# Performance work log

Measured on AMD Instinct MI355X. Metric: run time of the kernel, lower is better.

## Reference

```python
import jax, jax.numpy as jnp
import numpy as np
from jax import lax

CHAOS_R = 3.5699456
N_STEPS = 10


def setup_inputs() -> dict:
    key = jax.random.key(0)
    k1, k2, k3 = jax.random.split(key, 3)
    B, T, D = 256, 8192, 5
    x = jax.random.normal(k1, (B, T, D), dtype=jnp.float32)
    temple = jax.random.normal(k2, (4, 5), dtype=jnp.float32)
    breath_vector = jax.random.normal(k3, (5,), dtype=jnp.float32)
    return {"x": x, "temple": temple, "breath_vector": breath_vector}


def reference(x, temple, breath_vector):
    # x: (B, T, D) with D == 5
    B, T, D = x.shape

    # mirror_sequence: chaos logistic map on mean of x[0,0]
    seed = jnp.mod(jnp.mean(x[0, 0]), 1.0)
    chaos = CHAOS_R * seed * (1.0 - seed)
    mirrored = jnp.where(chaos > 0.7, 9.0 - x,
                         jnp.where(chaos > 0.4, jnp.flip(x, axis=1), x))
    mode_code = jnp.where(chaos > 0.7, 0, jnp.where(chaos > 0.4, 1, 2))  # 0=invert,1=retrograde,2=none

    extended_x = jnp.concatenate([x, mirrored], axis=1)  # (B, 2T, D)

    # per-token breath: first T tokens use breath[:4], mirrored half uses breath[1:5]
    breath_main = breath_vector[:4]
    breath_mirror = breath_vector[1:5]
    breath = jnp.concatenate([
        jnp.broadcast_to(breath_main, (T, 4)),
        jnp.broadcast_to(breath_mirror, (T, 4)),
    ], axis=0)  # (2T, 4)

    def step(vec, _):
        # vec: (B, 2T, 5)
        transformed = jnp.einsum('rd,btd->btr', temple, vec)  # (B, 2T, 4)
        resonance = jnp.sum(transformed * breath[None, :, :], axis=-1)  # (B, 2T)
        vec = jnp.roll(vec, shift=1, axis=-1).at[..., 0].set(jnp.mod(resonance, 10.0))
        return vec, resonance

    vec0 = extended_x[..., :5]
    _, history = lax.scan(step, vec0, None, length=N_STEPS)  # (10, B, 2T)

    # torch.std default is unbiased (ddof=1)
    score = 1.0 / (1.0 + jnp.std(history, axis=0, ddof=1))  # (B, 2T)
    gate_weights = score[..., None]  # (B, 2T, 1)
    return gate_weights, extended_x, mode_code
```

## Files before the change

### kernel.cpp

```cpp
#include <hip/hip_runtime.h>

#define NSTEPS 10
constexpr int B_DIM = 256, T_DIM = 8192, D_DIM = 5;
constexpr int TILE  = 1024;
constexpr int BLOCK = 256;
constexpr long long GATE_N = (long long)B_DIM * 2 * T_DIM;
constexpr long long EXT_N  = GATE_N * D_DIM;

__device__ __forceinline__ float scan_score(double v0, double v1, double v2, double v3, double v4,
                                            const double* __restrict__ w) {
    float h[NSTEPS];
#pragma unroll
    for (int s = 0; s < NSTEPS; ++s) {
        double res = v0 * w[0];
        res = fma(v1, w[1], res);
        res = fma(v2, w[2], res);
        res = fma(v3, w[3], res);
        res = fma(v4, w[4], res);
        h[s] = (float)res;
        double q = floor(res * 0.1);
        double m = fma(q, -10.0, res);
        m = (m < 0.0)   ? m + 10.0 : m;
        m = (m >= 10.0) ? m - 10.0 : m;
        v4 = v3; v3 = v2; v2 = v1; v1 = v0; v0 = m;
    }
    float mean = 0.f;
#pragma unroll
    for (int s = 0; s < NSTEPS; ++s) mean += h[s];
    mean *= 0.1f;
    float ssd = 0.f;
#pragma unroll
    for (int s = 0; s < NSTEPS; ++s) { float d = h[s] - mean; ssd = fmaf(d, d, ssd); }
    float sd = sqrtf(ssd * (1.0f / 9.0f));
    return 1.0f / (1.0f + sd);
}

__global__ __launch_bounds__(BLOCK) void temple_gate_kernel(
    const float* __restrict__ x, const float* __restrict__ temple,
    const float* __restrict__ breath, float* __restrict__ out) {
    __shared__ float lds[TILE * D_DIM];

    const int k  = threadIdx.x;
    const int b  = blockIdx.x >> 3;
    const int t0 = (blockIdx.x & 7) * TILE;

    double s = 0.0;
    for (int d = 0; d < 5; ++d) s += (double)x[d];
    s = s / 5.0;
    double seed  = s - floor(s);
    double chaos = 3.5699456 * seed * (1.0 - seed);
    const int mode = (chaos > 0.7) ? 0 : ((chaos > 0.4) ? 1 : 2);
    double wm[5], wx[5];
#pragma unroll
    for (int d = 0; d < 5; ++d) {
        double a = 0.0, c = 0.0;
#pragma unroll
        for (int r = 0; r < 4; ++r) {
            double tv = (double)temple[r * 5 + d];
            a += (double)breath[r]     * tv;
            c += (double)breath[r + 1] * tv;
        }
        wm[d] = a; wx[d] = c;
    }
    if (blockIdx.x == 0 && k == 0) out[GATE_N + EXT_N] = (float)mode;

    const long long srcBase = ((long long)b * T_DIM + t0) * D_DIM;
    const float4* __restrict__ src = (const float4*)(x + srcBase);
    float4 r0 = src[k],       r1 = src[k + 256], r2 = src[k + 512],
           r3 = src[k + 768], r4 = src[k + 1024];

    float4* l4 = (float4*)lds;
    l4[k] = r0; l4[k + 256] = r1; l4[k + 512] = r2; l4[k + 768] = r3; l4[k + 1024] = r4;

    float* gate = out;
    float* ext  = out + GATE_N;
    const long long rowBase = (long long)b * (2 * T_DIM);

    {
        float4* dst = (float4*)(ext + (rowBase + t0) * D_DIM);
        dst[k] = r0; dst[k + 256] = r1; dst[k + 512] = r2; dst[k + 768] = r3; dst[k + 1024] = r4;
    }
    if (mode == 0) {
        float4* dst = (float4*)(ext + (rowBase + T_DIM + t0) * D_DIM);
        float4 m0 = make_float4(9.f - r0.x, 9.f - r0.y, 9.f - r0.z, 9.f - r0.w);
        float4 m1 = make_float4(9.f - r1.x, 9.f - r1.y, 9.f - r1.z, 9.f - r1.w);
        float4 m2 = make_float4(9.f - r2.x, 9.f - r2.y, 9.f - r2.z, 9.f - r2.w);
        float4 m3 = make_float4(9.f - r3.x, 9.f - r3.y, 9.f - r3.z, 9.f - r3.w);
        float4 m4 = make_float4(9.f - r4.x, 9.f - r4.y, 9.f - r4.z, 9.f - r4.w);
        dst[k] = m0; dst[k + 256] = m1; dst[k + 512] = m2; dst[k + 768] = m3; dst[k + 1024] = m4;
    } else if (mode == 2) {
        float4* dst = (float4*)(ext + (rowBase + T_DIM + t0) * D_DIM);
        dst[k] = r0; dst[k + 256] = r1; dst[k + 512] = r2; dst[k + 768] = r3; dst[k + 1024] = r4;
    }

    __syncthreads();

    if (mode == 1) {
        float4* dst = (float4*)(ext + (rowBase + 2 * T_DIM - t0 - TILE) * D_DIM);
#pragma unroll
        for (int j = 0; j < 5; ++j) {
            const int q = k + j * 256;
            const int f = q * 4;
            float v[4];
#pragma unroll
            for (int c = 0; c < 4; ++c) {
                const int fc = f + c;
                const int fi = fc / 5, d = fc - fi * 5;
                v[c] = lds[(TILE - 1 - fi) * 5 + d];
            }
            dst[q] = make_float4(v[0], v[1], v[2], v[3]);
        }
    }

    {
        const int itBase = 4 * k;
        float gm[4], gx[4];
#pragma unroll
        for (int j = 0; j < 4; ++j) {
            const float* p = &lds[(itBase + j) * 5];
            double v0 = p[0], v1 = p[1], v2 = p[2], v3 = p[3], v4 = p[4];
            gm[j] = scan_score(v0, v1, v2, v3, v4, wm);
            if (mode == 0) { v0 = 9.0 - v0; v1 = 9.0 - v1; v2 = 9.0 - v2; v3 = 9.0 - v3; v4 = 9.0 - v4; }
            gx[j] = scan_score(v0, v1, v2, v3, v4, wx);
        }
        ((float4*)(gate + rowBase + t0))[k] = make_float4(gm[0], gm[1], gm[2], gm[3]);
        if (mode == 1) {
            ((float4*)(gate + rowBase + 2 * T_DIM - t0 - TILE))[255 - k] =
                make_float4(gx[3], gx[2], gx[1], gx[0]);
        } else {
            ((float4*)(gate + rowBase + T_DIM + t0))[k] = make_float4(gx[0], gx[1], gx[2], gx[3]);
        }
    }
}

extern "C" void kernel_launch(void* const* d_in, const int* in_sizes, int n_in,
                              void* d_out, int out_size, void* d_ws, size_t ws_size,
                              hipStream_t stream) {
    const float* x      = (const float*)d_in[0];
    const float* temple = (const float*)d_in[1];
    const float* breath = (const float*)d_in[2];
    float* out = (float*)d_out;

    const int blocks = (B_DIM * T_DIM) / TILE;
    temple_gate_kernel<<<blocks, BLOCK, 0, stream>>>(x, temple, breath, out);
}
```

Before: 145.4 us.

## Load each thread's own tokens into registers and skip LDS outside retrograde mode

Each thread now loads five consecutive float4s, which are exactly its four tokens, into registers, instead of strided float4s that were shuffled through LDS. The scan then reads its inputs directly from registers. LDS and the barrier are used only in retrograde mode, where the thread reads a mirrored thread's chunk and reverses token order before writing. The trade-off is that the global loads and stores become per-thread contiguous (stride 80 bytes across lanes) rather than perfectly coalesced, which may lower memory efficiency.

```diff
diff --git a/kernel.cpp b/kernel.cpp
--- a/kernel.cpp
+++ b/kernel.cpp
@@ -38,13 +38,14 @@
 __global__ __launch_bounds__(BLOCK) void temple_gate_kernel(
     const float* __restrict__ x, const float* __restrict__ temple,
     const float* __restrict__ breath, float* __restrict__ out) {
-    __shared__ float lds[TILE * D_DIM];
+    __shared__ float4 l4[TILE * D_DIM / 4];
 
     const int k  = threadIdx.x;
     const int b  = blockIdx.x >> 3;
     const int t0 = (blockIdx.x & 7) * TILE;
 
     double s = 0.0;
+#pragma unroll
     for (int d = 0; d < 5; ++d) s += (double)x[d];
     s = s / 5.0;
     double seed  = s - floor(s);
@@ -64,72 +65,69 @@
     }
     if (blockIdx.x == 0 && k == 0) out[GATE_N + EXT_N] = (float)mode;
 
-    const long long srcBase = ((long long)b * T_DIM + t0) * D_DIM;
-    const float4* __restrict__ src = (const float4*)(x + srcBase);
-    float4 r0 = src[k],       r1 = src[k + 256], r2 = src[k + 512],
-           r3 = src[k + 768], r4 = src[k + 1024];
-
-    float4* l4 = (float4*)lds;
-    l4[k] = r0; l4[k + 256] = r1; l4[k + 512] = r2; l4[k + 768] = r3; l4[k + 1024] = r4;
+    const float4* __restrict__ src = (const float4*)(x + ((long long)b * T_DIM + t0) * D_DIM);
+    float4 q[5];
+#pragma unroll
+    for (int j = 0; j < 5; ++j) q[j] = src[5 * k + j];
+    float f[20];
+#pragma unroll
+    for (int j = 0; j < 5; ++j) ((float4*)f)[j] = q[j];
 
     float* gate = out;
     float* ext  = out + GATE_N;
     const long long rowBase = (long long)b * (2 * T_DIM);
 
-    {
-        float4* dst = (float4*)(ext + (rowBase + t0) * D_DIM);
-        dst[k] = r0; dst[k + 256] = r1; dst[k + 512] = r2; dst[k + 768] = r3; dst[k + 1024] = r4;
-    }
-    if (mode == 0) {
-        float4* dst = (float4*)(ext + (rowBase + T_DIM + t0) * D_DIM);
-        float4 m0 = make_float4(9.f - r0.x, 9.f - r0.y, 9.f - r0.z, 9.f - r0.w);
-        float4 m1 = make_float4(9.f - r1.x, 9.f - r1.y, 9.f - r1.z, 9.f - r1.w);
-        float4 m2 = make_float4(9.f - r2.x, 9.f - r2.y, 9.f - r2.z, 9.f - r2.w);
-        float4 m3 = make_float4(9.f - r3.x, 9.f - r3.y, 9.f - r3.z, 9.f - r3.w);
-        float4 m4 = make_float4(9.f - r4.x, 9.f - r4.y, 9.f - r4.z, 9.f - r4.w);
-        dst[k] = m0; dst[k + 256] = m1; dst[k + 512] = m2; dst[k + 768] = m3; dst[k + 1024] = m4;
-    } else if (mode == 2) {
-        float4* dst = (float4*)(ext + (rowBase + T_DIM + t0) * D_DIM);
-        dst[k] = r0; dst[k + 256] = r1; dst[k + 512] = r2; dst[k + 768] = r3; dst[k + 1024] = r4;
-    }
-
-    __syncthreads();
-
     if (mode == 1) {
-        float4* dst = (float4*)(ext + (rowBase + 2 * T_DIM - t0 - TILE) * D_DIM);
 #pragma unroll
-        for (int j = 0; j < 5; ++j) {
-            const int q = k + j * 256;
-            const int f = q * 4;
-            float v[4];
-#pragma unroll
-            for (int c = 0; c < 4; ++c) {
-                const int fc = f + c;
-                const int fi = fc / 5, d = fc - fi * 5;
-                v[c] = lds[(TILE - 1 - fi) * 5 + d];
-            }
-            dst[q] = make_float4(v[0], v[1], v[2], v[3]);
-        }
+        for (int j = 0; j < 5; ++j) l4[5 * k + j] = q[j];
     }
 
     {
-        const int itBase = 4 * k;
-        float gm[4], gx[4];
+        float4* dst = (float4*)(ext + (rowBase + t0) * D_DIM);
 #pragma unroll
-        for (int j = 0; j < 4; ++j) {
-            const float* p = &lds[(itBase + j) * 5];
-            double v0 = p[0], v1 = p[1], v2 = p[2], v3 = p[3], v4 = p[4];
-            gm[j] = scan_score(v0, v1, v2, v3, v4, wm);
-            if (mode == 0) { v0 = 9.0 - v0; v1 = 9.0 - v1; v2 = 9.0 - v2; v3 = 9.0 - v3; v4 = 9.0 - v4; }
-            gx[j] = scan_score(v0, v1, v2, v3, v4, wx);
-        }
-        ((float4*)(gate + rowBase + t0))[k] = make_float4(gm[0], gm[1], gm[2], gm[3]);
-        if (mode == 1) {
-            ((float4*)(gate + rowBase + 2 * T_DIM - t0 - TILE))[255 - k] =
-                make_float4(gx[3], gx[2], gx[1], gx[0]);
-        } else {
-            ((float4*)(gate + rowBase + T_DIM + t0))[k] = make_float4(gx[0], gx[1], gx[2], gx[3]);
-        }
+        for (int j = 0; j < 5; ++j) dst[5 * k + j] = q[j];
+    }
+
+    if (mode == 0) {
+        float4* dst = (float4*)(ext + (rowBase + T_DIM + t0) * D_DIM);
+#pragma unroll
+        for (int j = 0; j < 5; ++j)
+            dst[5 * k + j] = make_float4(9.f - q[j].x, 9.f - q[j].y, 9.f - q[j].z, 9.f - q[j].w);
+    } else if (mode == 2) {
+        float4* dst = (float4*)(ext + (rowBase + T_DIM + t0) * D_DIM);
+#pragma unroll
+        for (int j = 0; j < 5; ++j) dst[5 * k + j] = q[j];
+    } else {
+        __syncthreads();
+        float pf[20];
+#pragma unroll
+        for (int j = 0; j < 5; ++j) ((float4*)pf)[j] = l4[5 * (255 - k) + j];
+        float df[20];
+#pragma unroll
+        for (int c = 0; c < 4; ++c)
+#pragma unroll
+            for (int d = 0; d < 5; ++d) df[c * 5 + d] = pf[(3 - c) * 5 + d];
+        float4* dst = (float4*)(ext + (rowBase + 2 * T_DIM - t0 - TILE) * D_DIM);
+#pragma unroll
+        for (int j = 0; j < 5; ++j)
+            dst[5 * k + j] = make_float4(df[4 * j], df[4 * j + 1], df[4 * j + 2], df[4 * j + 3]);
+    }
+
+    float gm[4], gx[4];
+#pragma unroll
+    for (int m = 0; m < 4; ++m) {
+        double v0 = f[m * 5 + 0], v1 = f[m * 5 + 1], v2 = f[m * 5 + 2],
+               v3 = f[m * 5 + 3], v4 = f[m * 5 + 4];
+        gm[m] = scan_score(v0, v1, v2, v3, v4, wm);
+        if (mode == 0) { v0 = 9.0 - v0; v1 = 9.0 - v1; v2 = 9.0 - v2; v3 = 9.0 - v3; v4 = 9.0 - v4; }
+        gx[m] = scan_score(v0, v1, v2, v3, v4, wx);
+    }
+    ((float4*)(gate + rowBase + t0))[k] = make_float4(gm[0], gm[1], gm[2], gm[3]);
+    if (mode == 1) {
+        ((float4*)(gate + rowBase + 2 * T_DIM - t0 - TILE))[255 - k] =
+            make_float4(gx[3], gx[2], gx[1], gx[0]);
+    } else {
+        ((float4*)(gate + rowBase + T_DIM + t0))[k] = make_float4(gx[0], gx[1], gx[2], gx[3]);
     }
 }
 
```

New measurement: 151.2 us. 4.0% more time.
